# Kernel optimization log

Measured on AMD Instinct MI355X. Metric: run time of the kernel, lower is better.

## Reference

```python
import jax, jax.numpy as jnp
import numpy as np

N_EMBD = 1024
N_HEAD = 16

def setup_inputs() -> dict:
    key = jax.random.key(0)
    k1, k2, k3 = jax.random.split(key, 3)
    x = jax.random.normal(k1, (2, 2048, N_EMBD), dtype=jnp.float32)
    # torch Linear(n, 3n): y = x @ W_attn (we store transposed weight directly)
    w_attn = jax.random.normal(k2, (N_EMBD, 3 * N_EMBD), dtype=jnp.float32) * 0.02
    w_proj = jax.random.normal(k3, (N_EMBD, N_EMBD), dtype=jnp.float32) * 0.02
    return {"x": x, "w_attn": w_attn, "w_proj": w_proj}

def reference(x, w_attn, w_proj):
    B, S, E = x.shape
    H = N_HEAD
    D = E // H
    qkv = x @ w_attn  # [B, S, 3E]
    q, k, v = jnp.split(qkv, 3, axis=-1)
    # [B, H, S, D]
    q = q.reshape(B, S, H, D).transpose(0, 2, 1, 3)
    k = k.reshape(B, S, H, D).transpose(0, 2, 1, 3)
    v = v.reshape(B, S, H, D).transpose(0, 2, 1, 3)
    scale = 1.0 / jnp.sqrt(jnp.asarray(D, dtype=x.dtype))
    a = jnp.einsum('bhqd,bhkd->bhqk', q, k) * scale  # [B, H, S, S]
    causal = jnp.tril(jnp.ones((S, S), dtype=bool))
    a = jnp.where(causal, a, -jnp.inf)
    a = jax.nn.softmax(a, axis=-1)
    y = jnp.einsum('bhqk,bhkd->bhqd', a, v)  # [B, H, S, D]
    y = y.transpose(0, 2, 1, 3).reshape(B, S, E)
    return y @ w_proj
```

## Files before the change

### kernel.cpp

```cpp
#include <hip/hip_runtime.h>

#define DEVI __device__ __forceinline__

typedef short bf16x8 __attribute__((ext_vector_type(8)));
typedef float f32x4 __attribute__((ext_vector_type(4)));
typedef unsigned short u16;
typedef unsigned int u32;

static constexpr int Bn = 2, S = 2048, E = 1024, H = 16, D = 64;
static constexpr int Mrows = Bn * S;
static constexpr int N_QKV = 3 * E;

DEVI u16 f2b(float f) {
  union { float f; u32 u; } c; c.f = f;
  return (u16)((c.u + 0x7FFFu + ((c.u >> 16) & 1u)) >> 16);
}

DEVI bf16x8 ld8(const u16* p) {
  union { uint4 u; bf16x8 v; } c;
  c.u = *reinterpret_cast<const uint4*>(p);
  return c.v;
}

#define MFMA(a, b, c) __builtin_amdgcn_mfma_f32_16x16x32_bf16(a, b, c, 0, 0, 0)

#define G2L16(gptr, lptr) \
  __builtin_amdgcn_global_load_lds((const __attribute__((address_space(1))) void*)(gptr), \
                                   (__attribute__((address_space(3))) void*)(lptr), 16, 0, 0)

__global__ __launch_bounds__(256) void prep(const float* __restrict__ x,
                                            const float* __restrict__ w_attn,
                                            const float* __restrict__ w_proj,
                                            u16* __restrict__ xb, u16* __restrict__ wabT,
                                            u16* __restrict__ wpbT) {
  __shared__ float t[32][33];
  int blk = blockIdx.x, tid = threadIdx.x;
  if (blk >= 4096) {
    int i = (blk - 4096) * 256 + tid;
    float4 f = reinterpret_cast<const float4*>(x)[i];
    ushort4 u;
    u.x = f2b(f.x); u.y = f2b(f.y); u.z = f2b(f.z); u.w = f2b(f.w);
    reinterpret_cast<ushort4*>(xb)[i] = u;
    return;
  }
  const float* in; u16* out; int R, C, bx, by;
  if (blk < 3072) {
    in = w_attn; out = wabT; R = E; C = N_QKV;
    bx = (blk % 96) * 32; by = (blk / 96) * 32;
  } else {
    int q = blk - 3072;
    in = w_proj; out = wpbT; R = E; C = E;
    bx = (q % 32) * 32; by = (q / 32) * 32;
  }
  int tx = tid & 31, ty = tid >> 5;
#pragma unroll
  for (int k = 0; k < 32; k += 8)
    t[ty + k][tx] = in[(size_t)(by + ty + k) * C + bx + tx];
  __syncthreads();
#pragma unroll
  for (int k = 0; k < 32; k += 8)
    out[(size_t)(bx + ty + k) * R + by + tx] = f2b(t[tx][ty + k]);
}

__global__ __launch_bounds__(256) void gemm_qkv(const u16* __restrict__ A, const u16* __restrict__ BT,
                                                u16* __restrict__ Qb, u16* __restrict__ Kb,
                                                u16* __restrict__ VbT) {
  constexpr int K = 1024, BK = 64;
  __shared__ __align__(16) u16 As[128 * BK];
  __shared__ __align__(16) u16 Bs[64 * BK];
  int tid = threadIdx.x;
  int w = tid >> 6, lane = tid & 63, quad = lane >> 4, l15 = lane & 15;
  int m0 = blockIdx.x * 128, n0 = blockIdx.y * 64;
  int mw = (w >> 1) * 64, nw = (w & 1) * 32;
  const bool qk = (n0 < 2048);
  const u16* Ab = A + (size_t)m0 * K;
  const u16* Bb = BT + (size_t)n0 * K;
  f32x4 acc[4][2] = {};
  for (int k0 = 0; k0 < K; k0 += BK) {
#pragma unroll
    for (int j = 0; j < 4; j++) {
      int L = j * 256 + tid;
      int row = L >> 3, cg = (L & 7) ^ (row & 7);
      G2L16(Ab + (size_t)row * K + k0 + cg * 8, (char*)As + L * 16);
    }
#pragma unroll
    for (int j = 0; j < 2; j++) {
      int L = j * 256 + tid;
      int row = L >> 3, cg = (L & 7) ^ (row & 7);
      G2L16(Bb + (size_t)row * K + k0 + cg * 8, (char*)Bs + L * 16);
    }
    __syncthreads();
#pragma unroll
    for (int kk = 0; kk < 2; kk++) {
      int sg = ((kk << 2) | quad) ^ (l15 & 7);
      bf16x8 a[4], b[2];
#pragma unroll
      for (int i = 0; i < 4; i++) a[i] = ld8(&As[(mw + i * 16 + l15) * BK + sg * 8]);
#pragma unroll
      for (int i = 0; i < 2; i++) b[i] = ld8(&Bs[(nw + i * 16 + l15) * BK + sg * 8]);
      if (qk) {
#pragma unroll
        for (int mb = 0; mb < 4; mb++)
#pragma unroll
          for (int nb = 0; nb < 2; nb++)
            acc[mb][nb] = MFMA(b[nb], a[mb], acc[mb][nb]);
      } else {
#pragma unroll
        for (int mb = 0; mb < 4; mb++)
#pragma unroll
          for (int nb = 0; nb < 2; nb++)
            acc[mb][nb] = MFMA(a[mb], b[nb], acc[mb][nb]);
      }
    }
    __syncthreads();
  }
  int h = (n0 & 1023) >> 6;
  if (qk) {
    int sec = n0 >> 10;
#pragma unroll
    for (int mb = 0; mb < 4; mb++) {
      int m = m0 + mw + mb * 16 + l15;
      int b = m >> 11, s = m & 2047;
      int bh = b * H + h;
      u16* dst = (sec == 0 ? Qb : Kb) + ((size_t)bh * S + s) * D;
#pragma unroll
      for (int nb = 0; nb < 2; nb++) {
        int d0 = nw + nb * 16 + quad * 4;
        ushort4 v;
        if (sec == 0) {
          v.x = f2b(acc[mb][nb][0] * 0.1803368801111244f);
          v.y = f2b(acc[mb][nb][1] * 0.1803368801111244f);
          v.z = f2b(acc[mb][nb][2] * 0.1803368801111244f);
          v.w = f2b(acc[mb][nb][3] * 0.1803368801111244f);
        } else {
          v.x = f2b(acc[mb][nb][0]); v.y = f2b(acc[mb][nb][1]);
          v.z = f2b(acc[mb][nb][2]); v.w = f2b(acc[mb][nb][3]);
        }
        *reinterpret_cast<ushort4*>(dst + d0) = v;
      }
    }
  } else {
#pragma unroll
    for (int mb = 0; mb < 4; mb++) {
      int m = m0 + mw + mb * 16 + quad * 4;
      int b = m >> 11, s = m & 2047;
      int bh = b * H + h;
#pragma unroll
      for (int nb = 0; nb < 2; nb++) {
        int d = nw + nb * 16 + l15;
        ushort4 v;
        v.x = f2b(acc[mb][nb][0]); v.y = f2b(acc[mb][nb][1]);
        v.z = f2b(acc[mb][nb][2]); v.w = f2b(acc[mb][nb][3]);
        *reinterpret_cast<ushort4*>(VbT + ((size_t)bh * D + d) * S + s) = v;
      }
    }
  }
}

__global__ __launch_bounds__(256, 3) void attn(const u16* __restrict__ Qb, const u16* __restrict__ Kb,
                                               const u16* __restrict__ VbT, u16* __restrict__ Yb) {
  __shared__ __align__(16) u16 Ks[128 * 64];
  __shared__ __align__(16) u16 Vs[64 * 128];
  __shared__ __align__(16) u32 Ps[4][16 * 68];
  int w = threadIdx.x >> 6, lane = threadIdx.x & 63, quad = lane >> 4, l15 = lane & 15;
  int bh = blockIdx.x & 31, qt = 31 - (blockIdx.x >> 5);
  int b = bh >> 4, h = bh & 15;
  int nc = (qt + 2) >> 1;

  const u16* Kbh = Kb + (size_t)bh * S * D;
  const u16* Vbh = VbT + (size_t)bh * D * S;
  u32* myP = &Ps[w][0];
  const u16* myP16 = (const u16*)myP;
  int prow = l15 * 68 + quad * 2;

  int q_base = qt * 64 + w * 16;
  int qrow = q_base + l15;
  int kmax = q_base + 16;

  const u16* Qp = Qb + ((size_t)bh * S + qrow) * D + quad * 8;
  bf16x8 bq0 = ld8(Qp), bq1 = ld8(Qp + 32);

  float lpart = 0.f;
  f32x4 o[4] = {};

  for (int c = 0; c < nc; c++) {
    int kbase = c * 128;
    __syncthreads();
    const u16* Kg = Kbh + (size_t)kbase * D;
#pragma unroll
    for (int j = 0; j < 4; j++) {
      int L = (w * 4 + j) * 64 + lane;
      int row = L >> 3, cg = (L & 7) ^ (row & 7);
      G2L16(Kg + (size_t)row * 64 + cg * 8, (char*)Ks + L * 16);
    }
    const u16* Vg = Vbh + kbase;
#pragma unroll
    for (int j = 0; j < 4; j++) {
      int L = (w * 4 + j) * 64 + lane;
      int row = L >> 4, cg = (L & 15) ^ (row & 15);
      G2L16(Vg + (size_t)row * S + cg * 8, (char*)Vs + L * 16);
    }
    __syncthreads();

#pragma unroll
    for (int mb = 0; mb < 8; mb++) {
      int kb = kbase + mb * 16;
      u32 pa = 0, pb = 0;
      if (kb < kmax) {
        int row = mb * 16 + l15;
        bf16x8 ak0 = ld8(&Ks[row * 64 + ((quad ^ (row & 7)) * 8)]);
        bf16x8 ak1 = ld8(&Ks[row * 64 + (((quad + 4) ^ (row & 7)) * 8)]);
        f32x4 z = {};
        z = MFMA(ak0, bq0, z);
        z = MFMA(ak1, bq1, z);
        if (kb == q_base) {
#pragma unroll
          for (int r = 0; r < 4; r++)
            if (quad * 4 + r > l15) z[r] = -1e30f;
        }
        float p0 = __builtin_amdgcn_exp2f(z[0]);
        float p1 = __builtin_amdgcn_exp2f(z[1]);
        float p2 = __builtin_amdgcn_exp2f(z[2]);
        float p3 = __builtin_amdgcn_exp2f(z[3]);
        lpart += (p0 + p1) + (p2 + p3);
        union { float f; u32 u; } c0, c1, c2, c3;
        c0.f = p0; c1.f = p1; c2.f = p2; c3.f = p3;
        pa = __builtin_amdgcn_perm(c1.u + 0x8000u, c0.u + 0x8000u, 0x07060302u);
        pb = __builtin_amdgcn_perm(c3.u + 0x8000u, c2.u + 0x8000u, 0x07060302u);
      }
      uint2 pw; pw.x = pa; pw.y = pb;
      *reinterpret_cast<uint2*>(&myP[prow + mb * 8]) = pw;
    }
#pragma unroll
    for (int ch = 0; ch < 4; ch++) {
      if (kbase + ch * 32 < kmax) {
        bf16x8 bp = ld8(myP16 + l15 * 136 + ch * 32 + quad * 8);
#pragma unroll
        for (int dd = 0; dd < 4; dd++) {
          int rv = dd * 16 + l15;
          bf16x8 av = ld8(&Vs[rv * 128 + (((ch * 4 + quad) ^ (rv & 15)) * 8)]);
          o[dd] = MFMA(av, bp, o[dd]);
        }
      }
    }
  }

  float l = lpart;
  l += __shfl_xor(l, 16);
  l += __shfl_xor(l, 32);
  float rinv = 1.0f / l;
  u16* Yp = Yb + ((size_t)b * S + qrow) * E + h * 64 + quad * 4;
#pragma unroll
  for (int dd = 0; dd < 4; dd++) {
    ushort4 y;
    y.x = f2b(o[dd][0] * rinv); y.y = f2b(o[dd][1] * rinv);
    y.z = f2b(o[dd][2] * rinv); y.w = f2b(o[dd][3] * rinv);
    *reinterpret_cast<ushort4*>(Yp + dd * 16) = y;
  }
}

__global__ __launch_bounds__(256) void gemm_proj(const u16* __restrict__ A, const u16* __restrict__ BT,
                                                 float* __restrict__ out) {
  constexpr int K = 1024, BK = 64;
  __shared__ __align__(16) u16 As[128 * BK];
  __shared__ __align__(16) u16 Bs[64 * BK];
  int tid = threadIdx.x;
  int w = tid >> 6, lane = tid & 63, quad = lane >> 4, l15 = lane & 15;
  int m0 = blockIdx.x * 128, n0 = blockIdx.y * 64;
  int mw = (w >> 1) * 64, nw = (w & 1) * 32;
  const u16* Ab = A + (size_t)m0 * K;
  const u16* Bb = BT + (size_t)n0 * K;
  f32x4 acc[4][2] = {};
  for (int k0 = 0; k0 < K; k0 += BK) {
#pragma unroll
    for (int j = 0; j < 4; j++) {
      int L = j * 256 + tid;
      int row = L >> 3, cg = (L & 7) ^ (row & 7);
      G2L16(Ab + (size_t)row * K + k0 + cg * 8, (char*)As + L * 16);
    }
#pragma unroll
    for (int j = 0; j < 2; j++) {
      int L = j * 256 + tid;
      int row = L >> 3, cg = (L & 7) ^ (row & 7);
      G2L16(Bb + (size_t)row * K + k0 + cg * 8, (char*)Bs + L * 16);
    }
    __syncthreads();
#pragma unroll
    for (int kk = 0; kk < 2; kk++) {
      int sg = ((kk << 2) | quad) ^ (l15 & 7);
      bf16x8 a[4], b[2];
#pragma unroll
      for (int i = 0; i < 4; i++) a[i] = ld8(&As[(mw + i * 16 + l15) * BK + sg * 8]);
#pragma unroll
      for (int i = 0; i < 2; i++) b[i] = ld8(&Bs[(nw + i * 16 + l15) * BK + sg * 8]);
#pragma unroll
      for (int mb = 0; mb < 4; mb++)
#pragma unroll
        for (int nb = 0; nb < 2; nb++)
          acc[mb][nb] = MFMA(b[nb], a[mb], acc[mb][nb]);
    }
    __syncthreads();
  }
#pragma unroll
  for (int mb = 0; mb < 4; mb++) {
    int m = m0 + mw + mb * 16 + l15;
#pragma unroll
    for (int nb = 0; nb < 2; nb++) {
      int n = n0 + nw + nb * 16 + quad * 4;
      float4 v;
      v.x = acc[mb][nb][0]; v.y = acc[mb][nb][1];
      v.z = acc[mb][nb][2]; v.w = acc[mb][nb][3];
      *reinterpret_cast<float4*>(&out[(size_t)m * E + n]) = v;
    }
  }
}

extern "C" void kernel_launch(void* const* d_in, const int* in_sizes, int n_in,
                              void* d_out, int out_size, void* d_ws, size_t ws_size,
                              hipStream_t stream) {
  const float* x = (const float*)d_in[0];
  const float* w_attn = (const float*)d_in[1];
  const float* w_proj = (const float*)d_in[2];
  float* out = (float*)d_out;
  char* ws = (char*)d_ws;

  u16* xb   = (u16*)(ws);
  u16* wabT = (u16*)(ws + 8388608);
  u16* wpbT = (u16*)(ws + 14680064);
  u16* Qb   = (u16*)(ws + 16777216);
  u16* Kb   = (u16*)(ws + 25165824);
  u16* VbT  = (u16*)(ws + 33554432);
  u16* Yb   = (u16*)(ws + 41943040);

  prep<<<8192, 256, 0, stream>>>(x, w_attn, w_proj, xb, wabT, wpbT);
  gemm_qkv<<<dim3(Mrows / 128, N_QKV / 64), 256, 0, stream>>>(xb, wabT, Qb, Kb, VbT);
  attn<<<Bn * H * (S / 64), 256, 0, stream>>>(Qb, Kb, VbT, Yb);
  gemm_proj<<<dim3(Mrows / 128, E / 64), 256, 0, stream>>>(Yb, wpbT, out);
}
```

Before: 168.2 us.

## Double-buffer QKV GEMM loads and keep attention probabilities in registers

```diff
diff --git a/kernel.cpp b/kernel.cpp
--- a/kernel.cpp
+++ b/kernel.cpp
@@ -65,9 +65,9 @@
 __global__ __launch_bounds__(256) void gemm_qkv(const u16* __restrict__ A, const u16* __restrict__ BT,
                                                 u16* __restrict__ Qb, u16* __restrict__ Kb,
                                                 u16* __restrict__ VbT) {
-  constexpr int K = 1024, BK = 64;
-  __shared__ __align__(16) u16 As[128 * BK];
-  __shared__ __align__(16) u16 Bs[64 * BK];
+  constexpr int K = 1024, BK = 64, NSTEP = K / BK;
+  __shared__ __align__(16) u16 As[2][128 * BK];
+  __shared__ __align__(16) u16 Bs[2][64 * BK];
   int tid = threadIdx.x;
   int w = tid >> 6, lane = tid & 63, quad = lane >> 4, l15 = lane & 15;
   int m0 = blockIdx.x * 128, n0 = blockIdx.y * 64;
@@ -76,28 +76,53 @@
   const u16* Ab = A + (size_t)m0 * K;
   const u16* Bb = BT + (size_t)n0 * K;
   f32x4 acc[4][2] = {};
-  for (int k0 = 0; k0 < K; k0 += BK) {
-#pragma unroll
-    for (int j = 0; j < 4; j++) {
-      int L = j * 256 + tid;
-      int row = L >> 3, cg = (L & 7) ^ (row & 7);
-      G2L16(Ab + (size_t)row * K + k0 + cg * 8, (char*)As + L * 16);
-    }
-#pragma unroll
-    for (int j = 0; j < 2; j++) {
-      int L = j * 256 + tid;
-      int row = L >> 3, cg = (L & 7) ^ (row & 7);
-      G2L16(Bb + (size_t)row * K + k0 + cg * 8, (char*)Bs + L * 16);
-    }
-    __syncthreads();
+
+#pragma unroll
+  for (int j = 0; j < 4; j++) {
+    int L = j * 256 + tid;
+    int row = L >> 3, cg = (L & 7) ^ (row & 7);
+    G2L16(Ab + (size_t)row * K + cg * 8, (char*)As[0] + L * 16);
+  }
+#pragma unroll
+  for (int j = 0; j < 2; j++) {
+    int L = j * 256 + tid;
+    int row = L >> 3, cg = (L & 7) ^ (row & 7);
+    G2L16(Bb + (size_t)row * K + cg * 8, (char*)Bs[0] + L * 16);
+  }
+
+  for (int s = 0; s < NSTEP; s++) {
+    int cur = s & 1;
+    if (s + 1 < NSTEP) {
+      int k1 = (s + 1) * BK;
+#pragma unroll
+      for (int j = 0; j < 4; j++) {
+        int L = j * 256 + tid;
+        int row = L >> 3, cg = (L & 7) ^ (row & 7);
+        G2L16(Ab + (size_t)row * K + k1 + cg * 8, (char*)As[cur ^ 1] + L * 16);
+      }
+#pragma unroll
+      for (int j = 0; j < 2; j++) {
+        int L = j * 256 + tid;
+        int row = L >> 3, cg = (L & 7) ^ (row & 7);
+        G2L16(Bb + (size_t)row * K + k1 + cg * 8, (char*)Bs[cur ^ 1] + L * 16);
+      }
+      asm volatile("s_waitcnt vmcnt(6)" ::: "memory");
+    } else {
+      asm volatile("s_waitcnt vmcnt(0)" ::: "memory");
+    }
+    __builtin_amdgcn_s_barrier();
+    __builtin_amdgcn_sched_barrier(0);
+
+    const u16* Asc = As[cur];
+    const u16* Bsc = Bs[cur];
 #pragma unroll
     for (int kk = 0; kk < 2; kk++) {
       int sg = ((kk << 2) | quad) ^ (l15 & 7);
       bf16x8 a[4], b[2];
 #pragma unroll
-      for (int i = 0; i < 4; i++) a[i] = ld8(&As[(mw + i * 16 + l15) * BK + sg * 8]);
-#pragma unroll
-      for (int i = 0; i < 2; i++) b[i] = ld8(&Bs[(nw + i * 16 + l15) * BK + sg * 8]);
+      for (int i = 0; i < 4; i++) a[i] = ld8(&Asc[(mw + i * 16 + l15) * BK + sg * 8]);
+#pragma unroll
+      for (int i = 0; i < 2; i++) b[i] = ld8(&Bsc[(nw + i * 16 + l15) * BK + sg * 8]);
       if (qk) {
 #pragma unroll
         for (int mb = 0; mb < 4; mb++)
@@ -112,17 +137,18 @@
             acc[mb][nb] = MFMA(a[mb], b[nb], acc[mb][nb]);
       }
     }
-    __syncthreads();
-  }
+    __builtin_amdgcn_s_barrier();
+  }
+
   int h = (n0 & 1023) >> 6;
   if (qk) {
     int sec = n0 >> 10;
 #pragma unroll
     for (int mb = 0; mb < 4; mb++) {
       int m = m0 + mw + mb * 16 + l15;
-      int b = m >> 11, s = m & 2047;
+      int b = m >> 11, ss = m & 2047;
       int bh = b * H + h;
-      u16* dst = (sec == 0 ? Qb : Kb) + ((size_t)bh * S + s) * D;
+      u16* dst = (sec == 0 ? Qb : Kb) + ((size_t)bh * S + ss) * D;
 #pragma unroll
       for (int nb = 0; nb < 2; nb++) {
         int d0 = nw + nb * 16 + quad * 4;
@@ -143,7 +169,7 @@
 #pragma unroll
     for (int mb = 0; mb < 4; mb++) {
       int m = m0 + mw + mb * 16 + quad * 4;
-      int b = m >> 11, s = m & 2047;
+      int b = m >> 11, ss = m & 2047;
       int bh = b * H + h;
 #pragma unroll
       for (int nb = 0; nb < 2; nb++) {
@@ -151,27 +177,26 @@
         ushort4 v;
         v.x = f2b(acc[mb][nb][0]); v.y = f2b(acc[mb][nb][1]);
         v.z = f2b(acc[mb][nb][2]); v.w = f2b(acc[mb][nb][3]);
-        *reinterpret_cast<ushort4*>(VbT + ((size_t)bh * D + d) * S + s) = v;
-      }
-    }
-  }
-}
-
-__global__ __launch_bounds__(256, 3) void attn(const u16* __restrict__ Qb, const u16* __restrict__ Kb,
+        *reinterpret_cast<ushort4*>(VbT + ((size_t)bh * D + d) * S + ss) = v;
+      }
+    }
+  }
+}
+
+__global__ __launch_bounds__(256, 4) void attn(const u16* __restrict__ Qb, const u16* __restrict__ Kb,
                                                const u16* __restrict__ VbT, u16* __restrict__ Yb) {
   __shared__ __align__(16) u16 Ks[128 * 64];
   __shared__ __align__(16) u16 Vs[64 * 128];
-  __shared__ __align__(16) u32 Ps[4][16 * 68];
   int w = threadIdx.x >> 6, lane = threadIdx.x & 63, quad = lane >> 4, l15 = lane & 15;
-  int bh = blockIdx.x & 31, qt = 31 - (blockIdx.x >> 5);
+  int bh = blockIdx.x & 31;
+  int g = blockIdx.x >> 5;
+  int ga = g & 7, gb = g >> 3;
+  int qt = ((gb & 2) << 3) + ((gb & 1) ? (15 - ga) : ga);
   int b = bh >> 4, h = bh & 15;
   int nc = (qt + 2) >> 1;
 
   const u16* Kbh = Kb + (size_t)bh * S * D;
   const u16* Vbh = VbT + (size_t)bh * D * S;
-  u32* myP = &Ps[w][0];
-  const u16* myP16 = (const u16*)myP;
-  int prow = l15 * 68 + quad * 2;
 
   int q_base = qt * 64 + w * 16;
   int qrow = q_base + l15;
@@ -203,44 +228,53 @@
     __syncthreads();
 
 #pragma unroll
-    for (int mb = 0; mb < 8; mb++) {
-      int kb = kbase + mb * 16;
-      u32 pa = 0, pb = 0;
-      if (kb < kmax) {
-        int row = mb * 16 + l15;
-        bf16x8 ak0 = ld8(&Ks[row * 64 + ((quad ^ (row & 7)) * 8)]);
-        bf16x8 ak1 = ld8(&Ks[row * 64 + (((quad + 4) ^ (row & 7)) * 8)]);
-        f32x4 z = {};
-        z = MFMA(ak0, bq0, z);
-        z = MFMA(ak1, bq1, z);
-        if (kb == q_base) {
-#pragma unroll
-          for (int r = 0; r < 4; r++)
-            if (quad * 4 + r > l15) z[r] = -1e30f;
+    for (int ch = 0; ch < 4; ch++) {
+      int kc = kbase + ch * 32;
+      if (kc < kmax) {
+        u32 pw0 = 0, pw1 = 0, pw2 = 0, pw3 = 0;
+#pragma unroll
+        for (int s = 0; s < 2; s++) {
+          int kb = kc + s * 16;
+          if (kb < kmax) {
+            int row = (ch * 2 + s) * 16 + l15;
+            bf16x8 ak0 = ld8(&Ks[row * 64 + ((quad ^ (row & 7)) * 8)]);
+            bf16x8 ak1 = ld8(&Ks[row * 64 + (((quad + 4) ^ (row & 7)) * 8)]);
+            f32x4 z = {};
+            __builtin_amdgcn_s_setprio(1);
+            z = MFMA(ak0, bq0, z);
+            z = MFMA(ak1, bq1, z);
+            __builtin_amdgcn_s_setprio(0);
+            if (kb == q_base) {
+#pragma unroll
+              for (int r = 0; r < 4; r++)
+                if (quad * 4 + r > l15) z[r] = -1e30f;
+            }
+            float p0 = __builtin_amdgcn_exp2f(z[0]);
+            float p1 = __builtin_amdgcn_exp2f(z[1]);
+            float p2 = __builtin_amdgcn_exp2f(z[2]);
+            float p3 = __builtin_amdgcn_exp2f(z[3]);
+            lpart += (p0 + p1) + (p2 + p3);
+            union { float f; u32 u; } c0, c1, c2, c3;
+            c0.f = p0; c1.f = p1; c2.f = p2; c3.f = p3;
+            u32 pa = __builtin_amdgcn_perm(c1.u + 0x8000u, c0.u + 0x8000u, 0x07060302u);
+            u32 pb = __builtin_amdgcn_perm(c3.u + 0x8000u, c2.u + 0x8000u, 0x07060302u);
+            if (s == 0) { pw0 = pa; pw1 = pb; } else { pw2 = pa; pw3 = pb; }
+          }
         }
-        float p0 = __builtin_amdgcn_exp2f(z[0]);
-        float p1 = __builtin_amdgcn_exp2f(z[1]);
-        float p2 = __builtin_amdgcn_exp2f(z[2]);
-        float p3 = __builtin_amdgcn_exp2f(z[3]);
-        lpart += (p0 + p1) + (p2 + p3);
-        union { float f; u32 u; } c0, c1, c2, c3;
-        c0.f = p0; c1.f = p1; c2.f = p2; c3.f = p3;
-        pa = __builtin_amdgcn_perm(c1.u + 0x8000u, c0.u + 0x8000u, 0x07060302u);
-        pb = __builtin_amdgcn_perm(c3.u + 0x8000u, c2.u + 0x8000u, 0x07060302u);
-      }
-      uint2 pw; pw.x = pa; pw.y = pb;
-      *reinterpret_cast<uint2*>(&myP[prow + mb * 8]) = pw;
-    }
-#pragma unroll
-    for (int ch = 0; ch < 4; ch++) {
-      if (kbase + ch * 32 < kmax) {
-        bf16x8 bp = ld8(myP16 + l15 * 136 + ch * 32 + quad * 8);
+        union { u32 u[4]; bf16x8 v; } bp;
+        bp.u[0] = pw0; bp.u[1] = pw1; bp.u[2] = pw2; bp.u[3] = pw3;
+        int cg0 = ch * 4 + (quad >> 1), cg1 = cg0 + 2;
+        int woff = (quad & 1) * 4;
+        __builtin_amdgcn_s_setprio(1);
 #pragma unroll
         for (int dd = 0; dd < 4; dd++) {
           int rv = dd * 16 + l15;
-          bf16x8 av = ld8(&Vs[rv * 128 + (((ch * 4 + quad) ^ (rv & 15)) * 8)]);
-          o[dd] = MFMA(av, bp, o[dd]);
+          union { uint2 d[2]; bf16x8 v; } av;
+          av.d[0] = *reinterpret_cast<const uint2*>(&Vs[rv * 128 + ((cg0 ^ (rv & 15)) * 8) + woff]);
+          av.d[1] = *reinterpret_cast<const uint2*>(&Vs[rv * 128 + ((cg1 ^ (rv & 15)) * 8) + woff]);
+          o[dd] = MFMA(av.v, bp.v, o[dd]);
         }
+        __builtin_amdgcn_s_setprio(0);
       }
     }
   }
```

Result: slower. 174.3 us (+3.6%).
